# Kernel tuning notes

Measured on AMD Instinct MI355X. Metric: run time of the kernel, lower is better.

## Reference

```python
import jax, jax.numpy as jnp
import numpy as np

TOP_K = 4
EPS = 1e-6


def setup_inputs() -> dict:
    key = jax.random.key(0)
    k1, k2, k3 = jax.random.split(key, 3)
    B, Q, N, H, W = 4, 200, 32, 256, 256
    pred_masks = jax.random.normal(k1, (B, Q, H, W), dtype=jnp.float32)
    pred_logits = jax.random.normal(k2, (B, Q, 2), dtype=jnp.float32)
    gt_masks = (jax.random.uniform(k3, (B, N, H, W)) < 0.3).astype(jnp.float32)
    return {"pred_masks": pred_masks, "pred_logits": pred_logits, "gt_masks": gt_masks}


def _combined_scores(pred_masks, pred_logits, gt_masks):
    """IoU * class-score, shape [B, Q, N]."""
    pm = jax.nn.sigmoid(pred_masks)                    # [B,Q,H,W]
    cls = jax.nn.softmax(pred_logits, axis=-1)[..., 1]  # [B,Q]
    B, Q = pm.shape[:2]
    N = gt_masks.shape[1]
    pmf = pm.reshape(B, Q, -1)                         # [B,Q,D]
    tmf = gt_masks.reshape(B, N, -1)                   # [B,N,D]
    inter = jnp.einsum('bqd,bnd->bqn', pmf, tmf)
    union = pmf.sum(-1)[:, :, None] + tmf.sum(-1)[:, None, :] - inter
    iou = inter / (union + EPS)
    return iou * cls[:, :, None]


def _greedy_assign(combined):
    """Greedy per-GT top-k with dedup. combined: [Q,N] -> sel indices [N,k], -1 = dropped."""
    Q = combined.shape[0]
    k = min(TOP_K, Q)

    def step(assigned, col):
        _, idx = jax.lax.top_k(col, k)          # [k] query indices for this GT
        taken = assigned[idx]                   # already assigned -> drop
        sel = jnp.where(taken, -1, idx)
        assigned = assigned.at[idx].set(True)
        return assigned, sel

    _, sels = jax.lax.scan(step, jnp.zeros(Q, dtype=bool), combined.T)
    return sels  # [N, k]


def reference(pred_masks, pred_logits, gt_masks):
    combined = _combined_scores(pred_masks, pred_logits, gt_masks)  # [B,Q,N]
    sels = jax.vmap(_greedy_assign)(combined)                       # [B,N,k]
    B, N, k = sels.shape
    src_idx = sels
    tgt_idx = jnp.broadcast_to(jnp.arange(N, dtype=jnp.int32)[None, :, None], sels.shape)
    valid = sels >= 0
    tgt_idx = jnp.where(valid, tgt_idx, -1)
    return src_idx, tgt_idx, valid
```

## Files before the change

### kernel.cpp

```cpp
#include <hip/hip_runtime.h>
#include <math.h>
#include <stdint.h>

#define BB    4
#define QQ    200
#define NGT   32
#define DD    65536
#define TOPK  4
#define EPSF  1e-6f
#define QP    208

#define QT16  13
#define KG    16
#define KSPAN (DD / KG)
#define KQ    (KSPAN / 4)
#define NIT   (KQ / 32)

typedef float  f32x4  __attribute__((ext_vector_type(4)));
typedef __bf16 bf16x8 __attribute__((ext_vector_type(8)));

__global__ __launch_bounds__(256) void k_pack(const float* __restrict__ gt,
                                              uint32_t* __restrict__ packed,
                                              float* __restrict__ zero_base) {
    int zidx = blockIdx.x * 256 + threadIdx.x;
    if (zidx < BB * NGT * QP + BB * QP) zero_base[zidx] = 0.0f;

    int blk = blockIdx.x;
    int b = blk >> 6;
    int d0 = ((blk & 63) * 256 + threadIdx.x) * 4;
    uint32_t px = 0, py = 0, pz = 0, pw = 0;
    const float* gb = gt + (size_t)b * NGT * DD + d0;
#pragma unroll
    for (int n = 0; n < NGT; ++n) {
        float4 g = *(const float4*)(gb + (size_t)n * DD);
        px |= (g.x > 0.5f ? 1u : 0u) << n;
        py |= (g.y > 0.5f ? 1u : 0u) << n;
        pz |= (g.z > 0.5f ? 1u : 0u) << n;
        pw |= (g.w > 0.5f ? 1u : 0u) << n;
    }
    *(uint4*)(packed + (size_t)b * DD + d0) = make_uint4(px, py, pz, pw);
}

__global__ __launch_bounds__(256) void k_tsum(const uint32_t* __restrict__ packed,
                                              float* __restrict__ tsum) {
    int b = blockIdx.x >> 5;
    int n = blockIdx.x & 31;
    const uint4* pp = (const uint4*)(packed + (size_t)b * DD);
    int cnt = 0;
    for (int i = threadIdx.x; i < DD / 4; i += 256) {
        uint4 w = pp[i];
        cnt += (int)((w.x >> n) & 1u) + (int)((w.y >> n) & 1u) +
               (int)((w.z >> n) & 1u) + (int)((w.w >> n) & 1u);
    }
#pragma unroll
    for (int off = 32; off; off >>= 1) cnt += __shfl_xor(cnt, off);
    __shared__ int red[4];
    if ((threadIdx.x & 63) == 0) red[threadIdx.x >> 6] = cnt;
    __syncthreads();
    if (threadIdx.x == 0)
        tsum[blockIdx.x] = (float)(red[0] + red[1] + red[2] + red[3]);
}

__global__ __launch_bounds__(256) void k_mfma(const float* __restrict__ pm,
                                              const uint32_t* __restrict__ packed,
                                              float* __restrict__ inter,
                                              float* __restrict__ psum) {
    int blk = blockIdx.x;
    int b   = blk / (QT16 * KG);
    int rem = blk % (QT16 * KG);
    int qt  = rem / KG;
    int kg  = rem % KG;
    int tid = threadIdx.x, lane = tid & 63, wave = tid >> 6;
    int m = lane & 15, quad = lane >> 4;

    int qg_m = qt * 16 + m;
    int qrow = qg_m < QQ ? qg_m : QQ - 1;

    const float*    ap = pm + ((size_t)b * QQ + qrow) * DD
                            + (size_t)kg * KSPAN + wave * KQ + quad * 8;
    const uint32_t* bp = packed + (size_t)b * DD
                                + (size_t)kg * KSPAN + wave * KQ + quad * 8;

    f32x4 cH0 = {0.f,0.f,0.f,0.f}, cL0 = {0.f,0.f,0.f,0.f};
    f32x4 cH1 = {0.f,0.f,0.f,0.f}, cL1 = {0.f,0.f,0.f,0.f};
    float ps = 0.f;

#pragma unroll 2
    for (int it = 0; it < NIT; ++it) {
        float4 a0 = *(const float4*)(ap + it * 32);
        float4 a1 = *(const float4*)(ap + it * 32 + 4);
        uint4  w0 = *(const uint4*)(bp + it * 32);
        uint4  w1 = *(const uint4*)(bp + it * 32 + 4);

        float xs[8] = {a0.x, a0.y, a0.z, a0.w, a1.x, a1.y, a1.z, a1.w};
        uint32_t hu[8], mu[8], lu[8];
#pragma unroll
        for (int i = 0; i < 8; ++i) {
            float x  = xs[i];
            float sg = __builtin_amdgcn_rcpf(1.0f + __expf(-x));
            ps += sg;
            uint32_t u0 = __float_as_uint(sg);
            float hi = __uint_as_float(u0 & 0xFFFF0000u);
            float r1 = sg - hi;
            uint32_t u1 = __float_as_uint(r1);
            float mi = __uint_as_float(u1 & 0xFFFF0000u);
            float r2 = r1 - mi;
            hu[i] = u0; mu[i] = u1; lu[i] = __float_as_uint(r2);
        }
        union { uint4 u; bf16x8 v; } ah, am, al;
        ah.u = make_uint4((hu[0] >> 16) | (hu[1] & 0xFFFF0000u),
                          (hu[2] >> 16) | (hu[3] & 0xFFFF0000u),
                          (hu[4] >> 16) | (hu[5] & 0xFFFF0000u),
                          (hu[6] >> 16) | (hu[7] & 0xFFFF0000u));
        am.u = make_uint4((mu[0] >> 16) | (mu[1] & 0xFFFF0000u),
                          (mu[2] >> 16) | (mu[3] & 0xFFFF0000u),
                          (mu[4] >> 16) | (mu[5] & 0xFFFF0000u),
                          (mu[6] >> 16) | (mu[7] & 0xFFFF0000u));
        al.u = make_uint4((lu[0] >> 16) | (lu[1] & 0xFFFF0000u),
                          (lu[2] >> 16) | (lu[3] & 0xFFFF0000u),
                          (lu[4] >> 16) | (lu[5] & 0xFFFF0000u),
                          (lu[6] >> 16) | (lu[7] & 0xFFFF0000u));

        uint32_t wj[8] = {w0.x, w0.y, w0.z, w0.w, w1.x, w1.y, w1.z, w1.w};
        union { ushort u[8]; bf16x8 v; } b0, b1;
#pragma unroll
        for (int j = 0; j < 8; ++j) {
            b0.u[j] = (ushort)((((int)(wj[j] << (31 - m))) >> 31) & 0x3F80);
            b1.u[j] = (ushort)((((int)(wj[j] << (15 - m))) >> 31) & 0x3F80);
        }

        cH0 = __builtin_amdgcn_mfma_f32_16x16x32_bf16(ah.v, b0.v, cH0, 0, 0, 0);
        cL0 = __builtin_amdgcn_mfma_f32_16x16x32_bf16(am.v, b0.v, cL0, 0, 0, 0);
        cL0 = __builtin_amdgcn_mfma_f32_16x16x32_bf16(al.v, b0.v, cL0, 0, 0, 0);
        cH1 = __builtin_amdgcn_mfma_f32_16x16x32_bf16(ah.v, b1.v, cH1, 0, 0, 0);
        cL1 = __builtin_amdgcn_mfma_f32_16x16x32_bf16(am.v, b1.v, cL1, 0, 0, 0);
        cL1 = __builtin_amdgcn_mfma_f32_16x16x32_bf16(al.v, b1.v, cL1, 0, 0, 0);
    }

    ps += __shfl_xor(ps, 16);
    ps += __shfl_xor(ps, 32);
    if (lane < 16) {
        int qg = qt * 16 + m;
        if (qg < QQ) atomicAdd(&psum[b * QP + qg], ps);
    }

    __shared__ float cred[3 * 64 * 9];
    float c8[8];
#pragma unroll
    for (int r = 0; r < 4; ++r) {
        c8[r]     = cH0[r] + cL0[r];
        c8[4 + r] = cH1[r] + cL1[r];
    }
    __syncthreads();
    if (wave > 0) {
        float* dst = cred + ((wave - 1) * 64 + lane) * 9;
#pragma unroll
        for (int r = 0; r < 8; ++r) dst[r] = c8[r];
    }
    __syncthreads();
    if (wave == 0) {
#pragma unroll
        for (int wv = 0; wv < 3; ++wv) {
            const float* sp = cred + (wv * 64 + lane) * 9;
#pragma unroll
            for (int r = 0; r < 8; ++r) c8[r] += sp[r];
        }
#pragma unroll
        for (int r = 0; r < 4; ++r) {
            int qg = qt * 16 + quad * 4 + r;
            if (qg < QQ) {
                atomicAdd(&inter[(b * NGT + m) * QP + qg],      c8[r]);
                atomicAdd(&inter[(b * NGT + 16 + m) * QP + qg], c8[4 + r]);
            }
        }
    }
}

__global__ __launch_bounds__(64) void k_topk(const float* __restrict__ inter,
                                             const float* __restrict__ psum,
                                             const float* __restrict__ tsum,
                                             const float* __restrict__ logits,
                                             int* __restrict__ idx4) {
    int bn = blockIdx.x;
    int b  = bn >> 5;
    int lane = threadIdx.x;
    float tsn = tsum[bn];
    float v[4];
#pragma unroll
    for (int s = 0; s < 4; ++s) {
        int q = lane + 64 * s;
        if (q < QQ) {
            float iv = inter[(size_t)bn * QP + q];
            float un = psum[b * QP + q] + tsn - iv;
            float l0 = logits[(b * QQ + q) * 2];
            float l1 = logits[(b * QQ + q) * 2 + 1];
            float cl = 1.0f / (1.0f + expf(l0 - l1));
            v[s] = iv / (un + EPSF) * cl;
        } else {
            v[s] = -INFINITY;
        }
    }
    for (int k = 0; k < TOPK; ++k) {
        float bv = -INFINITY;
        int   bi = 0x7fffffff;
#pragma unroll
        for (int s = 0; s < 4; ++s)
            if (v[s] > bv) { bv = v[s]; bi = lane + 64 * s; }
#pragma unroll
        for (int off = 32; off; off >>= 1) {
            float ov = __shfl_xor(bv, off);
            int   oi = __shfl_xor(bi, off);
            if (ov > bv || (ov == bv && oi < bi)) { bv = ov; bi = oi; }
        }
        if (lane == (bi & 63)) v[bi >> 6] = -INFINITY;
        if (lane == 0) idx4[bn * TOPK + k] = bi;
    }
}

__global__ __launch_bounds__(64) void k_final(const int* __restrict__ idx4,
                                              int* __restrict__ out) {
    int b = blockIdx.x;
    int lane = threadIdx.x;
    int* src = out;
    int* tgt = out + BB * NGT * TOPK;
    int* val = out + 2 * BB * NGT * TOPK;
    int asg = 0;
    for (int n = 0; n < NGT; ++n) {
        int4 id = *(const int4*)&idx4[(b * NGT + n) * TOPK];
        int ids[4] = {id.x, id.y, id.z, id.w};
        int newasg = asg;
#pragma unroll
        for (int k = 0; k < TOPK; ++k) {
            int idx = ids[k];
            int owner = idx & 63, slot = idx >> 6;
            int oasg = __shfl(asg, owner);
            int taken = (oasg >> slot) & 1;
            if (lane == owner) newasg |= (1 << slot);
            if (lane == 0) {
                int o = (b * NGT + n) * TOPK + k;
                src[o] = taken ? -1 : idx;
                tgt[o] = taken ? -1 : n;
                val[o] = taken ? 0 : 1;
            }
        }
        asg = newasg;
    }
}

extern "C" void kernel_launch(void* const* d_in, const int* in_sizes, int n_in,
                              void* d_out, int out_size, void* d_ws, size_t ws_size,
                              hipStream_t stream) {
    const float* pred_masks  = (const float*)d_in[0];
    const float* pred_logits = (const float*)d_in[1];
    const float* gt_masks    = (const float*)d_in[2];

    uint8_t* ws = (uint8_t*)d_ws;
    uint32_t* packed = (uint32_t*)ws;
    float* tsum  = (float*)(ws + (size_t)BB * DD * 4);
    float* inter = tsum + BB * NGT;
    float* psum  = inter + BB * NGT * QP;
    int*   idx4  = (int*)(psum + BB * QP);

    k_pack <<<BB * (DD / 1024), 256, 0, stream>>>(gt_masks, packed, inter);
    k_tsum <<<BB * NGT,         256, 0, stream>>>(packed, tsum);
    k_mfma <<<BB * QT16 * KG,   256, 0, stream>>>(pred_masks, packed, inter, psum);
    k_topk <<<BB * NGT,          64, 0, stream>>>(inter, psum, tsum, pred_logits, idx4);
    k_final<<<BB,                64, 0, stream>>>(idx4, (int*)d_out);
}
```

Before: 362.1 us.

## Fuse topk and greedy kernels, double K-split grid, use byte-perm packing

Merges the per-GT top-k kernel and the greedy dedup kernel into one per-batch kernel that keeps the top-k indices in shared memory, removing one launch and a global round trip. It doubles the K-split factor of the MFMA kernel so more blocks run in parallel, at the cost of more atomic adds into the intersection buffer. It also replaces the shift/mask bf16 packing and the bit-to-bf16 expansion with v_perm byte permutes and a multiply trick to cut ALU instructions per iteration. The fused match kernel runs on only four blocks, which serialises the top-k work per batch.

```diff
diff --git a/kernel.cpp b/kernel.cpp
--- a/kernel.cpp
+++ b/kernel.cpp
@@ -11,13 +11,16 @@
 #define QP    208
 
 #define QT16  13
-#define KG    16
+#define KG    32
 #define KSPAN (DD / KG)
 #define KQ    (KSPAN / 4)
 #define NIT   (KQ / 32)
 
 typedef float  f32x4  __attribute__((ext_vector_type(4)));
 typedef __bf16 bf16x8 __attribute__((ext_vector_type(8)));
+
+#define PERM_HI16 0x07060302u
+#define PERM_LO16 0x05040100u
 
 __global__ __launch_bounds__(256) void k_pack(const float* __restrict__ gt,
                                               uint32_t* __restrict__ packed,
@@ -108,26 +111,35 @@
             hu[i] = u0; mu[i] = u1; lu[i] = __float_as_uint(r2);
         }
         union { uint4 u; bf16x8 v; } ah, am, al;
-        ah.u = make_uint4((hu[0] >> 16) | (hu[1] & 0xFFFF0000u),
-                          (hu[2] >> 16) | (hu[3] & 0xFFFF0000u),
-                          (hu[4] >> 16) | (hu[5] & 0xFFFF0000u),
-                          (hu[6] >> 16) | (hu[7] & 0xFFFF0000u));
-        am.u = make_uint4((mu[0] >> 16) | (mu[1] & 0xFFFF0000u),
-                          (mu[2] >> 16) | (mu[3] & 0xFFFF0000u),
-                          (mu[4] >> 16) | (mu[5] & 0xFFFF0000u),
-                          (mu[6] >> 16) | (mu[7] & 0xFFFF0000u));
-        al.u = make_uint4((lu[0] >> 16) | (lu[1] & 0xFFFF0000u),
-                          (lu[2] >> 16) | (lu[3] & 0xFFFF0000u),
-                          (lu[4] >> 16) | (lu[5] & 0xFFFF0000u),
-                          (lu[6] >> 16) | (lu[7] & 0xFFFF0000u));
+        ah.u = make_uint4(__builtin_amdgcn_perm(hu[1], hu[0], PERM_HI16),
+                          __builtin_amdgcn_perm(hu[3], hu[2], PERM_HI16),
+                          __builtin_amdgcn_perm(hu[5], hu[4], PERM_HI16),
+                          __builtin_amdgcn_perm(hu[7], hu[6], PERM_HI16));
+        am.u = make_uint4(__builtin_amdgcn_perm(mu[1], mu[0], PERM_HI16),
+                          __builtin_amdgcn_perm(mu[3], mu[2], PERM_HI16),
+                          __builtin_amdgcn_perm(mu[5], mu[4], PERM_HI16),
+                          __builtin_amdgcn_perm(mu[7], mu[6], PERM_HI16));
+        al.u = make_uint4(__builtin_amdgcn_perm(lu[1], lu[0], PERM_HI16),
+                          __builtin_amdgcn_perm(lu[3], lu[2], PERM_HI16),
+                          __builtin_amdgcn_perm(lu[5], lu[4], PERM_HI16),
+                          __builtin_amdgcn_perm(lu[7], lu[6], PERM_HI16));
 
         uint32_t wj[8] = {w0.x, w0.y, w0.z, w0.w, w1.x, w1.y, w1.z, w1.w};
-        union { ushort u[8]; bf16x8 v; } b0, b1;
+        uint32_t ob[8];
 #pragma unroll
         for (int j = 0; j < 8; ++j) {
-            b0.u[j] = (ushort)((((int)(wj[j] << (31 - m))) >> 31) & 0x3F80);
-            b1.u[j] = (ushort)((((int)(wj[j] << (15 - m))) >> 31) & 0x3F80);
-        }
+            uint32_t t = wj[j] >> m;
+            ob[j] = (t & 0x10001u) * 0x3F80u;
+        }
+        union { uint4 u; bf16x8 v; } b0, b1;
+        b0.u = make_uint4(__builtin_amdgcn_perm(ob[1], ob[0], PERM_LO16),
+                          __builtin_amdgcn_perm(ob[3], ob[2], PERM_LO16),
+                          __builtin_amdgcn_perm(ob[5], ob[4], PERM_LO16),
+                          __builtin_amdgcn_perm(ob[7], ob[6], PERM_LO16));
+        b1.u = make_uint4(__builtin_amdgcn_perm(ob[1], ob[0], PERM_HI16),
+                          __builtin_amdgcn_perm(ob[3], ob[2], PERM_HI16),
+                          __builtin_amdgcn_perm(ob[5], ob[4], PERM_HI16),
+                          __builtin_amdgcn_perm(ob[7], ob[6], PERM_HI16));
 
         cH0 = __builtin_amdgcn_mfma_f32_16x16x32_bf16(ah.v, b0.v, cH0, 0, 0, 0);
         cL0 = __builtin_amdgcn_mfma_f32_16x16x32_bf16(am.v, b0.v, cL0, 0, 0, 0);
@@ -176,74 +188,76 @@
     }
 }
 
-__global__ __launch_bounds__(64) void k_topk(const float* __restrict__ inter,
-                                             const float* __restrict__ psum,
-                                             const float* __restrict__ tsum,
-                                             const float* __restrict__ logits,
-                                             int* __restrict__ idx4) {
-    int bn = blockIdx.x;
-    int b  = bn >> 5;
-    int lane = threadIdx.x;
-    float tsn = tsum[bn];
-    float v[4];
-#pragma unroll
-    for (int s = 0; s < 4; ++s) {
-        int q = lane + 64 * s;
-        if (q < QQ) {
-            float iv = inter[(size_t)bn * QP + q];
-            float un = psum[b * QP + q] + tsn - iv;
-            float l0 = logits[(b * QQ + q) * 2];
-            float l1 = logits[(b * QQ + q) * 2 + 1];
-            float cl = 1.0f / (1.0f + expf(l0 - l1));
-            v[s] = iv / (un + EPSF) * cl;
-        } else {
-            v[s] = -INFINITY;
-        }
-    }
-    for (int k = 0; k < TOPK; ++k) {
-        float bv = -INFINITY;
-        int   bi = 0x7fffffff;
-#pragma unroll
-        for (int s = 0; s < 4; ++s)
-            if (v[s] > bv) { bv = v[s]; bi = lane + 64 * s; }
-#pragma unroll
-        for (int off = 32; off; off >>= 1) {
-            float ov = __shfl_xor(bv, off);
-            int   oi = __shfl_xor(bi, off);
-            if (ov > bv || (ov == bv && oi < bi)) { bv = ov; bi = oi; }
-        }
-        if (lane == (bi & 63)) v[bi >> 6] = -INFINITY;
-        if (lane == 0) idx4[bn * TOPK + k] = bi;
-    }
-}
-
-__global__ __launch_bounds__(64) void k_final(const int* __restrict__ idx4,
-                                              int* __restrict__ out) {
+__global__ __launch_bounds__(256) void k_match(const float* __restrict__ inter,
+                                               const float* __restrict__ psum,
+                                               const float* __restrict__ tsum,
+                                               const float* __restrict__ logits,
+                                               int* __restrict__ out) {
     int b = blockIdx.x;
-    int lane = threadIdx.x;
-    int* src = out;
-    int* tgt = out + BB * NGT * TOPK;
-    int* val = out + 2 * BB * NGT * TOPK;
-    int asg = 0;
-    for (int n = 0; n < NGT; ++n) {
-        int4 id = *(const int4*)&idx4[(b * NGT + n) * TOPK];
-        int ids[4] = {id.x, id.y, id.z, id.w};
-        int newasg = asg;
-#pragma unroll
+    int tid = threadIdx.x, lane = tid & 63, wave = tid >> 6;
+    __shared__ int sidx[NGT][TOPK];
+
+    for (int nn = 0; nn < 8; ++nn) {
+        int n  = wave * 8 + nn;
+        int bn = b * NGT + n;
+        float tsn = tsum[bn];
+        float v[4];
+#pragma unroll
+        for (int s = 0; s < 4; ++s) {
+            int q = lane + 64 * s;
+            if (q < QQ) {
+                float iv = inter[(size_t)bn * QP + q];
+                float un = psum[b * QP + q] + tsn - iv;
+                float l0 = logits[(b * QQ + q) * 2];
+                float l1 = logits[(b * QQ + q) * 2 + 1];
+                float cl = 1.0f / (1.0f + expf(l0 - l1));
+                v[s] = iv / (un + EPSF) * cl;
+            } else {
+                v[s] = -INFINITY;
+            }
+        }
         for (int k = 0; k < TOPK; ++k) {
-            int idx = ids[k];
-            int owner = idx & 63, slot = idx >> 6;
-            int oasg = __shfl(asg, owner);
-            int taken = (oasg >> slot) & 1;
-            if (lane == owner) newasg |= (1 << slot);
-            if (lane == 0) {
-                int o = (b * NGT + n) * TOPK + k;
-                src[o] = taken ? -1 : idx;
-                tgt[o] = taken ? -1 : n;
-                val[o] = taken ? 0 : 1;
-            }
-        }
-        asg = newasg;
+            float bv = -INFINITY;
+            int   bi = 0x7fffffff;
+#pragma unroll
+            for (int s = 0; s < 4; ++s)
+                if (v[s] > bv) { bv = v[s]; bi = lane + 64 * s; }
+#pragma unroll
+            for (int off = 32; off; off >>= 1) {
+                float ov = __shfl_xor(bv, off);
+                int   oi = __shfl_xor(bi, off);
+                if (ov > bv || (ov == bv && oi < bi)) { bv = ov; bi = oi; }
+            }
+            if (lane == (bi & 63)) v[bi >> 6] = -INFINITY;
+            if (lane == 0) sidx[n][k] = bi;
+        }
+    }
+    __syncthreads();
+
+    if (wave == 0) {
+        int* src = out;
+        int* tgt = out + BB * NGT * TOPK;
+        int* val = out + 2 * BB * NGT * TOPK;
+        int asg = 0;
+        for (int n = 0; n < NGT; ++n) {
+            int ids[4] = {sidx[n][0], sidx[n][1], sidx[n][2], sidx[n][3]};
+            int newasg = asg;
+#pragma unroll
+            for (int k = 0; k < TOPK; ++k) {
+                int idx = ids[k];
+                int owner = idx & 63, slot = idx >> 6;
+                int oasg = __shfl(asg, owner);
+                int taken = (oasg >> slot) & 1;
+                if (lane == owner) newasg |= (1 << slot);
+                if (lane == 0) {
+                    int o = (b * NGT + n) * TOPK + k;
+                    src[o] = taken ? -1 : idx;
+                    tgt[o] = taken ? -1 : n;
+                    val[o] = taken ? 0 : 1;
+                }
+            }
+            asg = newasg;
+        }
     }
 }
 
@@ -259,11 +273,9 @@
     float* tsum  = (float*)(ws + (size_t)BB * DD * 4);
     float* inter = tsum + BB * NGT;
     float* psum  = inter + BB * NGT * QP;
-    int*   idx4  = (int*)(psum + BB * QP);
 
     k_pack <<<BB * (DD / 1024), 256, 0, stream>>>(gt_masks, packed, inter);
     k_tsum <<<BB * NGT,         256, 0, stream>>>(packed, tsum);
     k_mfma <<<BB * QT16 * KG,   256, 0, stream>>>(pred_masks, packed, inter, psum);
-    k_topk <<<BB * NGT,          64, 0, stream>>>(inter, psum, tsum, pred_logits, idx4);
-    k_final<<<BB,                64, 0, stream>>>(idx4, (int*)d_out);
-}
+    k_match<<<BB,               256, 0, stream>>>(inter, psum, tsum, pred_logits, (int*)d_out);
+}
```

New measurement: 364.7 us. No clear change (+0.7%).
